# Kernel tuning notes

Hardware: AMD Instinct MI355X
Metric: run time of the kernel (lower is better)

The kernel has to match this reference:

```python
import jax, jax.numpy as jnp
import numpy as np
import math

D_MODEL, N_HEAD, N_KV_HEAD, MAX_LEN = 2048, 32, 8, 2048
D_K = D_MODEL // N_HEAD
BASE = 10000.0
B, T = 2, 2048


def _rope_tables(seq_len):
    # matches torch Rotary: cos/sin of shape [seq_len, D_K], repeat_interleave(2) over freq dim
    inv_freq = 1.0 / (BASE ** (jnp.arange(0, D_K, 2, dtype=jnp.float32) / D_K))
    t = jnp.arange(seq_len, dtype=jnp.float32)[:, None] * inv_freq  # [T, D_K/2]
    cos = jnp.repeat(jnp.cos(t), 2, axis=-1)  # [T, D_K]
    sin = jnp.repeat(jnp.sin(t), 2, axis=-1)
    return cos, sin


def _rotate_half(x):
    # faithful to source: x1 = even lanes, x2 = odd lanes, concat([-x2, x1], -1)
    x1, x2 = x[..., ::2], x[..., 1::2]
    return jnp.concatenate([-x2, x1], axis=-1)


def _apply_rope(x, cos, sin):
    return x * cos + _rotate_half(x) * sin


def setup_inputs() -> dict:
    key = jax.random.key(0)
    ks = jax.random.split(key, 5)
    s = 1.0 / math.sqrt(D_MODEL)
    x = jax.random.normal(ks[0], (B, T, D_MODEL), dtype=jnp.float32)
    Wq = jax.random.normal(ks[1], (D_MODEL, N_HEAD * D_K), dtype=jnp.float32) * s
    Wk = jax.random.normal(ks[2], (D_MODEL, N_KV_HEAD * D_K), dtype=jnp.float32) * s
    Wv = jax.random.normal(ks[3], (D_MODEL, N_KV_HEAD * D_K), dtype=jnp.float32) * s
    Wo = jax.random.normal(ks[4], (N_HEAD * D_K, D_MODEL), dtype=jnp.float32) * s
    mask = jnp.tril(jnp.ones((T, T), dtype=bool))  # causal
    return {"x": x, "mask": mask, "Wq": Wq, "Wk": Wk, "Wv": Wv, "Wo": Wo}


def reference(x, mask, Wq, Wk, Wv, Wo):
    b, t, _ = x.shape
    g = N_HEAD // N_KV_HEAD
    q = (x @ Wq).reshape(b, t, N_HEAD, D_K).transpose(0, 2, 1, 3)      # [B,H,T,d]
    k = (x @ Wk).reshape(b, t, N_KV_HEAD, D_K).transpose(0, 2, 1, 3)   # [B,Hkv,T,d]
    v = (x @ Wv).reshape(b, t, N_KV_HEAD, D_K).transpose(0, 2, 1, 3)
    cos, sin = _rope_tables(t)
    q = _apply_rope(q, cos, sin)
    k = _apply_rope(k, cos, sin)  # rope before/after repeat is identical per-head
    # grouped attention: q head h attends kv head h // g (repeat_interleave semantics)
    qg = q.reshape(b, N_KV_HEAD, g, t, D_K)
    scores = jnp.einsum("bkgtd,bksd->bkgts", qg, k) / math.sqrt(D_K)
    neg = jnp.finfo(scores.dtype).min
    scores = jnp.where(mask[None, None, None, :, :], scores, neg)
    attn = jax.nn.softmax(scores, axis=-1)
    out = jnp.einsum("bkgts,bksd->bkgtd", attn, v)
    out = out.reshape(b, N_HEAD, t, D_K).transpose(0, 2, 1, 3).reshape(b, t, N_HEAD * D_K)
    return out @ Wo
```

## Files before the change

kernel.cpp:

```cpp
#include <hip/hip_runtime.h>
#include <cstdint>
#include <cstddef>

typedef unsigned short u16;
typedef __attribute__((ext_vector_type(8))) short bf16x8;
typedef __attribute__((ext_vector_type(8))) unsigned short u16x8;
typedef __attribute__((ext_vector_type(4))) unsigned short u16x4;
typedef __attribute__((ext_vector_type(4))) float f32x4;

__device__ __forceinline__ unsigned short f2bf(float f) {
    union { float f; uint32_t u; } c; c.f = f;
    uint32_t u = c.u + 0x7fffu + ((c.u >> 16) & 1u);
    return (unsigned short)(u >> 16);
}
__device__ __forceinline__ float bf2f(unsigned short h) {
    union { uint32_t u; float f; } c; c.u = ((uint32_t)h) << 16;
    return c.f;
}
__device__ __forceinline__ uint32_t pkbf(float a, float b) {
    union { float f; uint32_t u; } x, y; x.f = a; y.f = b;
    return ((x.u + 0x8000u) >> 16) | ((y.u + 0x8000u) & 0xFFFF0000u);
}
__device__ __forceinline__ uint32_t cvtpk(float a, float b) {
    uint32_t r;
    asm("v_cvt_pk_bf16_f32 %0, %1, %2" : "=v"(r) : "v"(a), "v"(b));
    return r;
}

#define GLDS16(g, l)                                                               \
    __builtin_amdgcn_global_load_lds((const __attribute__((address_space(1))) void*)(g), \
                                     (__attribute__((address_space(3))) void*)(l), 16, 0, 0)

__global__ __launch_bounds__(256) void cvt_x(const float* __restrict__ src,
                                             u16* __restrict__ dst) {
    int i = blockIdx.x * 256 + threadIdx.x;
    const float4* s = (const float4*)src + (size_t)i * 2;
    float4 a = s[0], b = s[1];
    u16x8 o;
    o[0] = f2bf(a.x); o[1] = f2bf(a.y); o[2] = f2bf(a.z); o[3] = f2bf(a.w);
    o[4] = f2bf(b.x); o[5] = f2bf(b.y); o[6] = f2bf(b.z); o[7] = f2bf(b.w);
    *(u16x8*)(dst + (size_t)i * 8) = o;
}

__global__ __launch_bounds__(256) void tcvt(const float* __restrict__ src,
                                            u16* __restrict__ dst, int C) {
    __shared__ u16 tile[32][33];
    const int t = threadIdx.x;
    const int bx = blockIdx.x, by = blockIdx.y;
    const int tr = t >> 3, tc = (t & 7) << 2;
    float4 f = *(const float4*)&src[(size_t)(by * 32 + tr) * C + bx * 32 + tc];
    tile[tr][tc + 0] = f2bf(f.x); tile[tr][tc + 1] = f2bf(f.y);
    tile[tr][tc + 2] = f2bf(f.z); tile[tr][tc + 3] = f2bf(f.w);
    __syncthreads();
    u16x4 o;
    o[0] = tile[tc + 0][tr]; o[1] = tile[tc + 1][tr];
    o[2] = tile[tc + 2][tr]; o[3] = tile[tc + 3][tr];
    *(u16x4*)&dst[(size_t)(bx * 32 + tr) * 2048 + by * 32 + tc] = o;
}

__global__ __launch_bounds__(256) void tcvt3(const float* __restrict__ Wq,
                                             const float* __restrict__ Wk,
                                             const float* __restrict__ Wv,
                                             u16* __restrict__ dst) {
    __shared__ u16 tile[32][33];
    const int t = threadIdx.x;
    const int bxg = blockIdx.x, by = blockIdx.y;
    const float* src; int C, nb; u16* dbase;
    if (bxg < 64)      { src = Wq; C = 2048; nb = bxg;      dbase = dst; }
    else if (bxg < 80) { src = Wk; C = 512;  nb = bxg - 64; dbase = dst + (size_t)2048 * 2048; }
    else               { src = Wv; C = 512;  nb = bxg - 80; dbase = dst + (size_t)2560 * 2048; }
    const int tr = t >> 3, tc = (t & 7) << 2;
    float4 f = *(const float4*)&src[(size_t)(by * 32 + tr) * C + nb * 32 + tc];
    tile[tr][tc + 0] = f2bf(f.x); tile[tr][tc + 1] = f2bf(f.y);
    tile[tr][tc + 2] = f2bf(f.z); tile[tr][tc + 3] = f2bf(f.w);
    __syncthreads();
    u16x4 o;
    o[0] = tile[tc + 0][tr]; o[1] = tile[tc + 1][tr];
    o[2] = tile[tc + 2][tr]; o[3] = tile[tc + 3][tr];
    *(u16x4*)&dbase[(size_t)(nb * 32 + tr) * 2048 + by * 32 + tc] = o;
}

template <int MODE>
__global__ __launch_bounds__(256) void gemm2(const u16* __restrict__ A,
                                             const u16* __restrict__ Bt,
                                             u16* __restrict__ oq, u16* __restrict__ ok,
                                             u16* __restrict__ ov, float* __restrict__ of) {
    __shared__ u16 As[128 * 32];
    __shared__ u16 Bs[128 * 32];
    const int t = threadIdx.x, w = t >> 6, lane = t & 63;
    const int l15 = lane & 15, quad = lane >> 4;
    const int m0 = blockIdx.y << 7, n0 = blockIdx.x << 7;
    const int K = 2048;
    const int c0 = w * 2, c1 = c0 + 1;
    const int ar0 = c0 * 16 + (lane >> 2), ar1 = c1 * 16 + (lane >> 2);
    const int ac = (lane & 3) << 3;
    const u16* Ap0 = A + (size_t)(m0 + ar0) * K + ac;
    const u16* Ap1 = A + (size_t)(m0 + ar1) * K + ac;
    const u16* Bp0 = Bt + (size_t)(n0 + ar0) * K + ac;
    const u16* Bp1 = Bt + (size_t)(n0 + ar1) * K + ac;
    const int wm = (w >> 1) << 6, wn = (w & 1) << 6;

    f32x4 acc[4][4] = {};

    for (int k0 = 0; k0 < K; k0 += 32) {
        GLDS16(Ap0 + k0, &As[c0 * 512]);
        GLDS16(Ap1 + k0, &As[c1 * 512]);
        GLDS16(Bp0 + k0, &Bs[c0 * 512]);
        GLDS16(Bp1 + k0, &Bs[c1 * 512]);
        __syncthreads();
        bf16x8 a[4], bfr[4];
#pragma unroll
        for (int mt = 0; mt < 4; ++mt)
            a[mt] = *(bf16x8*)&As[(wm + mt * 16 + l15) * 32 + quad * 8];
#pragma unroll
        for (int nt = 0; nt < 4; ++nt)
            bfr[nt] = *(bf16x8*)&Bs[(wn + nt * 16 + l15) * 32 + quad * 8];
#pragma unroll
        for (int mt = 0; mt < 4; ++mt)
#pragma unroll
            for (int nt = 0; nt < 4; ++nt)
                acc[mt][nt] = __builtin_amdgcn_mfma_f32_16x16x32_bf16(a[mt], bfr[nt], acc[mt][nt], 0, 0, 0);
        __syncthreads();
    }

    if constexpr (MODE == 0) {
        const int colbase = n0 + wn;
        const bool isv = (colbase >= 2560);
        float iv[4];
        if (!isv) {
#pragma unroll
            for (int nt = 0; nt < 4; ++nt)
                iv[nt] = exp2f(-0.4152410118609253f * (float)(nt * 8 + (l15 >> 1)));
        }
        const int map1 = (quad << 4) | ((2 * l15 + 1) & 15);
        const int map2 = (quad << 4) | ((2 * l15) & 15);
        const bool lo = (l15 < 8);
#pragma unroll
        for (int mt = 0; mt < 4; ++mt)
#pragma unroll
            for (int r = 0; r < 4; ++r) {
                const int row = m0 + wm + mt * 16 + quad * 4 + r;
                float v0 = acc[mt][0][r], v1 = acc[mt][1][r];
                float v2 = acc[mt][2][r], v3 = acc[mt][3][r];
                float o0 = v0, o1 = v1, o2 = v2, o3 = v3;
                if (!isv) {
                    float g1a = __shfl(v0, map1), g1b = __shfl(v1, map1);
                    float g1c = __shfl(v2, map1), g1d = __shfl(v3, map1);
                    float g2a = __shfl(v0, map2), g2b = __shfl(v1, map2);
                    float g2c = __shfl(v2, map2), g2d = __shfl(v3, map2);
                    float p0 = lo ? g1a : g1b;
                    float p1 = lo ? g1c : g1d;
                    float p2 = lo ? g2a : g2b;
                    float p3 = lo ? g2c : g2d;
                    const float tt = (float)(row & 2047);
                    float sn, cs;
                    __sincosf(tt * iv[0], &sn, &cs); o0 = v0 * cs - p0 * sn;
                    __sincosf(tt * iv[1], &sn, &cs); o1 = v1 * cs - p1 * sn;
                    __sincosf(tt * iv[2], &sn, &cs); o2 = v2 * cs + p2 * sn;
                    __sincosf(tt * iv[3], &sn, &cs); o3 = v3 * cs + p3 * sn;
                }
                float o[4] = {o0, o1, o2, o3};
                if (colbase < 2048) {
#pragma unroll
                    for (int nt = 0; nt < 4; ++nt)
                        oq[(size_t)row * 2048 + colbase + nt * 16 + l15] = f2bf(o[nt]);
                } else if (colbase < 2560) {
#pragma unroll
                    for (int nt = 0; nt < 4; ++nt)
                        ok[(size_t)row * 512 + colbase - 2048 + nt * 16 + l15] = f2bf(o[nt]);
                } else {
#pragma unroll
                    for (int nt = 0; nt < 4; ++nt)
                        ov[(size_t)(colbase - 2560 + nt * 16 + l15) * 4096 + row] = f2bf(o[nt]);
                }
            }
    } else {
#pragma unroll
        for (int mt = 0; mt < 4; ++mt)
#pragma unroll
            for (int nt = 0; nt < 4; ++nt)
#pragma unroll
                for (int r = 0; r < 4; ++r) {
                    int row = m0 + wm + mt * 16 + quad * 4 + r;
                    int col = n0 + wn + nt * 16 + l15;
                    of[(size_t)row * 2048 + col] = acc[mt][nt][r];
                }
    }
}

__global__ __launch_bounds__(256, 2) void attn5(const u16* __restrict__ q,
                                                const u16* __restrict__ k,
                                                const u16* __restrict__ vT,
                                                u16* __restrict__ att) {
    __shared__ u16 Ks[64 * 72];
    __shared__ u16 Vt[64 * 72];
    __shared__ u16 Pw[4][2][2][16 * 72];

    const int t = threadIdx.x, w = t >> 6, lane = t & 63;
    const int l15 = lane & 15, quad = lane >> 4;
    const int x = blockIdx.x, kvh = blockIdx.y, z = blockIdx.z;
    const int a = z ? (31 - x) : x;
    const int h = kvh * 4 + w;
    const size_t rowbase = (size_t)z * 2048;
    const int sr = t >> 2, sd = (t & 3) << 4;
    const float SC = 0.125f * 1.4426950408889634f;

    const u16* kbase = &k[(rowbase + sr) * 512 + kvh * 64 + sd];
    const u16* vbase = &vT[(size_t)(kvh * 64 + sr) * 4096 + rowbase + sd];

    const int ntiles = a + 1;
    const int qbase0 = a * 64;

    bf16x8 aq[2][2][2];
#pragma unroll
    for (int g = 0; g < 2; ++g)
#pragma unroll
        for (int m = 0; m < 2; ++m)
#pragma unroll
            for (int kc = 0; kc < 2; ++kc)
                aq[g][m][kc] = *(const bf16x8*)&q[(rowbase + qbase0 + g * 32 + m * 16 + l15) * 2048 +
                                                  h * 64 + kc * 32 + quad * 8];

    f32x4 acc[2][2][4] = {};
    float m_i[2][2] = {{-INFINITY, -INFINITY}, {-INFINITY, -INFINITY}};
    float l_i[2][2] = {{0.f, 0.f}, {0.f, 0.f}};

    u16x8 pk0 = *(const u16x8*)kbase;
    u16x8 pk1 = *(const u16x8*)(kbase + 8);
    u16x8 pv0 = *(const u16x8*)vbase;
    u16x8 pv1 = *(const u16x8*)(vbase + 8);

    for (int kb = 0; kb < ntiles; ++kb) {
        __syncthreads();
        *(u16x8*)&Ks[sr * 72 + sd]     = pk0;
        *(u16x8*)&Ks[sr * 72 + sd + 8] = pk1;
        *(u16x8*)&Vt[sr * 72 + sd]     = pv0;
        *(u16x8*)&Vt[sr * 72 + sd + 8] = pv1;
        if (kb + 1 < ntiles) {
            const u16* kp = kbase + (size_t)(kb + 1) * 64 * 512;
            pk0 = *(const u16x8*)kp;
            pk1 = *(const u16x8*)(kp + 8);
            const u16* vp = vbase + (size_t)(kb + 1) * 64;
            pv0 = *(const u16x8*)vp;
            pv1 = *(const u16x8*)(vp + 8);
        }
        __syncthreads();

        f32x4 st[2][2][4] = {};
#pragma unroll
        for (int kt = 0; kt < 4; ++kt) {
            bf16x8 ak0 = *(bf16x8*)&Ks[(kt * 16 + l15) * 72 + quad * 8];
            bf16x8 ak1 = *(bf16x8*)&Ks[(kt * 16 + l15) * 72 + 32 + quad * 8];
#pragma unroll
            for (int g = 0; g < 2; ++g)
#pragma unroll
                for (int m = 0; m < 2; ++m) {
                    st[g][m][kt] = __builtin_amdgcn_mfma_f32_16x16x32_bf16(ak0, aq[g][m][0], st[g][m][kt], 0, 0, 0);
                    st[g][m][kt] = __builtin_amdgcn_mfma_f32_16x16x32_bf16(ak1, aq[g][m][1], st[g][m][kt], 0, 0, 0);
                }
        }
        const bool diag = (kb == ntiles - 1);

        float alpha_[2][2];
        bool  resc[2][2];
#pragma unroll
        for (int g = 0; g < 2; ++g)
#pragma unroll
            for (int m = 0; m < 2; ++m) {
                float sv[16];
#pragma unroll
                for (int kt = 0; kt < 4; ++kt)
#pragma unroll
                    for (int r = 0; r < 4; ++r) sv[kt * 4 + r] = st[g][m][kt][r];
                if (diag) {
                    const int qg = qbase0 + g * 32 + m * 16 + l15;
#pragma unroll
                    for (int kt = 0; kt < 4; ++kt)
#pragma unroll
                        for (int r = 0; r < 4; ++r) {
                            int key = kb * 64 + kt * 16 + quad * 4 + r;
                            if (key > qg) sv[kt * 4 + r] = -INFINITY;
                        }
                }
                float mx = sv[0];
#pragma unroll
                for (int i = 1; i < 16; ++i) mx = fmaxf(mx, sv[i]);
                mx = fmaxf(mx, __shfl_xor(mx, 16));
                mx = fmaxf(mx, __shfl_xor(mx, 32));
                mx *= SC;
                const float mold = m_i[g][m];
                const bool need = __any(mx > mold + 8.f);
                float al = 1.f;
                if (need) {
                    const float mnew = fmaxf(mold, mx);
                    al = __builtin_amdgcn_exp2f(mold - mnew);
                    m_i[g][m] = mnew;
                }
                const float mu = m_i[g][m];
                float sum = 0.f;
#pragma unroll
                for (int i = 0; i < 16; ++i) {
                    sv[i] = __builtin_amdgcn_exp2f(fmaf(sv[i], SC, -mu));
                    sum += sv[i];
                }
                sum += __shfl_xor(sum, 16);
                sum += __shfl_xor(sum, 32);
                l_i[g][m] = l_i[g][m] * al + sum;
                alpha_[g][m] = al;
                resc[g][m] = need;

                u16* Pq = &Pw[w][g][m][0];
#pragma unroll
                for (int kt = 0; kt < 4; ++kt) {
                    uint2 uu;
                    uu.x = cvtpk(sv[kt * 4 + 0], sv[kt * 4 + 1]);
                    uu.y = cvtpk(sv[kt * 4 + 2], sv[kt * 4 + 3]);
                    *(uint2*)&Pq[l15 * 72 + kt * 16 + quad * 4] = uu;
                }
            }

#pragma unroll
        for (int g = 0; g < 2; ++g)
#pragma unroll
            for (int m = 0; m < 2; ++m)
                if (resc[g][m]) {
                    const float al = alpha_[g][m];
#pragma unroll
                    for (int dt = 0; dt < 4; ++dt)
#pragma unroll
                        for (int r = 0; r < 4; ++r) acc[g][m][dt][r] *= al;
                }

        bf16x8 bp[2][2][2];
#pragma unroll
        for (int g = 0; g < 2; ++g)
#pragma unroll
            for (int m = 0; m < 2; ++m) {
                const u16* Pq = &Pw[w][g][m][0];
                bp[g][m][0] = *(bf16x8*)&Pq[l15 * 72 + quad * 8];
                bp[g][m][1] = *(bf16x8*)&Pq[l15 * 72 + 32 + quad * 8];
            }

#pragma unroll
        for (int dt = 0; dt < 4; ++dt) {
            bf16x8 av0 = *(bf16x8*)&Vt[(dt * 16 + l15) * 72 + quad * 8];
            bf16x8 av1 = *(bf16x8*)&Vt[(dt * 16 + l15) * 72 + 32 + quad * 8];
#pragma unroll
            for (int g = 0; g < 2; ++g)
#pragma unroll
                for (int m = 0; m < 2; ++m) {
                    acc[g][m][dt] = __builtin_amdgcn_mfma_f32_16x16x32_bf16(av0, bp[g][m][0], acc[g][m][dt], 0, 0, 0);
                    acc[g][m][dt] = __builtin_amdgcn_mfma_f32_16x16x32_bf16(av1, bp[g][m][1], acc[g][m][dt], 0, 0, 0);
                }
        }
    }

#pragma unroll
    for (int g = 0; g < 2; ++g)
#pragma unroll
        for (int m = 0; m < 2; ++m) {
            float inv = 1.0f / l_i[g][m];
            size_t row = rowbase + qbase0 + g * 32 + m * 16 + l15;
#pragma unroll
            for (int dt = 0; dt < 4; ++dt) {
                uint2 uu;
                uu.x = cvtpk(acc[g][m][dt][0] * inv, acc[g][m][dt][1] * inv);
                uu.y = cvtpk(acc[g][m][dt][2] * inv, acc[g][m][dt][3] * inv);
                *(uint2*)&att[row * 2048 + h * 64 + dt * 16 + quad * 4] = uu;
            }
        }
}

extern "C" void kernel_launch(void* const* d_in, const int* in_sizes, int n_in,
                              void* d_out, int out_size, void* d_ws, size_t ws_size,
                              hipStream_t stream) {
    const float* x  = (const float*)d_in[0];
    const float* Wq = (const float*)d_in[2];
    const float* Wk = (const float*)d_in[3];
    const float* Wv = (const float*)d_in[4];
    const float* Wo = (const float*)d_in[5];
    float* out = (float*)d_out;

    u16* xb = (u16*)d_out;

    u16* q     = (u16*)d_ws;
    u16* kk    = q + (size_t)4096 * 2048;
    u16* vt    = kk + (size_t)4096 * 512;
    u16* wqkvt = vt + (size_t)4096 * 512;
    u16* att   = wqkvt;
    u16* wot   = kk;

    cvt_x<<<4096, 256, 0, stream>>>(x, xb);
    tcvt3<<<dim3(96, 64), 256, 0, stream>>>(Wq, Wk, Wv, wqkvt);
    gemm2<0><<<dim3(24, 32), 256, 0, stream>>>(xb, wqkvt, q, kk, vt, nullptr);
    attn5<<<dim3(32, 8, 2), 256, 0, stream>>>(q, kk, vt, att);
    tcvt<<<dim3(64, 64), 256, 0, stream>>>(Wo, wot, 2048);
    gemm2<1><<<dim3(16, 32), 256, 0, stream>>>(att, wot, nullptr, nullptr, nullptr, out);
}
```

Baseline: 331.4 us.

## Double-buffer K/V in attention with 8 waves, XOR-swizzled LDS and MFMA priority

The attention kernel now runs 512 threads per block, so 8 waves each own 32 query rows instead of 4 waves owning 64. K/V tiles go into double-buffered LDS, and the next tile is stored during softmax, which drops one barrier per iteration. Padded 72-stride LDS rows are replaced by 64-wide rows with an XOR swizzle to avoid bank conflicts, and s_setprio raises priority around the MFMA sections. Per-wave register use falls, allowing more resident waves, at the cost of more LDS per block and more Q loads per block.

```diff
diff --git a/kernel.cpp b/kernel.cpp
--- a/kernel.cpp
+++ b/kernel.cpp
@@ -16,10 +16,6 @@
 __device__ __forceinline__ float bf2f(unsigned short h) {
     union { uint32_t u; float f; } c; c.u = ((uint32_t)h) << 16;
     return c.f;
-}
-__device__ __forceinline__ uint32_t pkbf(float a, float b) {
-    union { float f; uint32_t u; } x, y; x.f = a; y.f = b;
-    return ((x.u + 0x8000u) >> 16) | ((y.u + 0x8000u) & 0xFFFF0000u);
 }
 __device__ __forceinline__ uint32_t cvtpk(float a, float b) {
     uint32_t r;
@@ -188,187 +184,187 @@
     }
 }
 
-__global__ __launch_bounds__(256, 2) void attn5(const u16* __restrict__ q,
+__global__ __launch_bounds__(512, 4) void attn6(const u16* __restrict__ q,
                                                 const u16* __restrict__ k,
                                                 const u16* __restrict__ vT,
                                                 u16* __restrict__ att) {
-    __shared__ u16 Ks[64 * 72];
-    __shared__ u16 Vt[64 * 72];
-    __shared__ u16 Pw[4][2][2][16 * 72];
+    __shared__ u16 Ks[2][64 * 64];
+    __shared__ u16 Vt[2][64 * 64];
+    __shared__ u16 Pw[8][2][16 * 64];
 
     const int t = threadIdx.x, w = t >> 6, lane = t & 63;
     const int l15 = lane & 15, quad = lane >> 4;
     const int x = blockIdx.x, kvh = blockIdx.y, z = blockIdx.z;
     const int a = z ? (31 - x) : x;
-    const int h = kvh * 4 + w;
+    const int h = kvh * 4 + (w & 3);
+    const int gw = w >> 2;
     const size_t rowbase = (size_t)z * 2048;
-    const int sr = t >> 2, sd = (t & 3) << 4;
     const float SC = 0.125f * 1.4426950408889634f;
-
-    const u16* kbase = &k[(rowbase + sr) * 512 + kvh * 64 + sd];
-    const u16* vbase = &vT[(size_t)(kvh * 64 + sr) * 4096 + rowbase + sd];
+    const int swz = l15 & 7;
+
+    const int srow = t >> 3;
+    const int slot = t & 7;
+    const int sd = slot << 3;
+    const int lidx = srow * 64 + ((slot ^ (srow & 7)) << 3);
+
+    const u16* kbase = &k[(rowbase + srow) * 512 + kvh * 64 + sd];
+    const u16* vbase = &vT[(size_t)(kvh * 64 + srow) * 4096 + rowbase + sd];
 
     const int ntiles = a + 1;
-    const int qbase0 = a * 64;
-
-    bf16x8 aq[2][2][2];
-#pragma unroll
-    for (int g = 0; g < 2; ++g)
+    const int qrow0 = a * 64 + gw * 32;
+
+    bf16x8 aq[2][2];
+#pragma unroll
+    for (int m = 0; m < 2; ++m)
+#pragma unroll
+        for (int kc = 0; kc < 2; ++kc)
+            aq[m][kc] = *(const bf16x8*)&q[(rowbase + qrow0 + m * 16 + l15) * 2048 +
+                                           h * 64 + kc * 32 + quad * 8];
+
+    f32x4 acc[2][4] = {};
+    float m_i[2] = {-INFINITY, -INFINITY};
+    float l_i[2] = {0.f, 0.f};
+
+    u16x8 pk = *(const u16x8*)kbase;
+    u16x8 pv = *(const u16x8*)vbase;
+    *(u16x8*)&Ks[0][lidx] = pk;
+    *(u16x8*)&Vt[0][lidx] = pv;
+    if (ntiles > 1) {
+        pk = *(const u16x8*)(kbase + (size_t)64 * 512);
+        pv = *(const u16x8*)(vbase + 64);
+    }
+    __syncthreads();
+
+    for (int kb = 0; kb < ntiles; ++kb) {
+        const int cur = kb & 1;
+        const u16* KsC = &Ks[cur][0];
+        const u16* VtC = &Vt[cur][0];
+
+        f32x4 st[2][4] = {};
+        __builtin_amdgcn_s_setprio(1);
+#pragma unroll
+        for (int kt = 0; kt < 4; ++kt) {
+            bf16x8 ak0 = *(const bf16x8*)&KsC[(kt * 16 + l15) * 64 + ((quad ^ swz) << 3)];
+            bf16x8 ak1 = *(const bf16x8*)&KsC[(kt * 16 + l15) * 64 + (((quad + 4) ^ swz) << 3)];
+#pragma unroll
+            for (int m = 0; m < 2; ++m) {
+                st[m][kt] = __builtin_amdgcn_mfma_f32_16x16x32_bf16(ak0, aq[m][0], st[m][kt], 0, 0, 0);
+                st[m][kt] = __builtin_amdgcn_mfma_f32_16x16x32_bf16(ak1, aq[m][1], st[m][kt], 0, 0, 0);
+            }
+        }
+        __builtin_amdgcn_s_setprio(0);
+
+        const bool diag = (kb == ntiles - 1);
+        float alpha_[2];
+        bool resc[2];
+#pragma unroll
+        for (int m = 0; m < 2; ++m) {
+            float sv[16];
+#pragma unroll
+            for (int kt = 0; kt < 4; ++kt)
+#pragma unroll
+                for (int r = 0; r < 4; ++r) sv[kt * 4 + r] = st[m][kt][r];
+            if (diag) {
+                const int qg = qrow0 + m * 16 + l15;
+#pragma unroll
+                for (int kt = 0; kt < 4; ++kt)
+#pragma unroll
+                    for (int r = 0; r < 4; ++r) {
+                        int key = kb * 64 + kt * 16 + quad * 4 + r;
+                        if (key > qg) sv[kt * 4 + r] = -INFINITY;
+                    }
+            }
+            float mx = sv[0];
+#pragma unroll
+            for (int i = 1; i < 16; ++i) mx = fmaxf(mx, sv[i]);
+            mx = fmaxf(mx, __shfl_xor(mx, 16));
+            mx = fmaxf(mx, __shfl_xor(mx, 32));
+            mx *= SC;
+            const float mold = m_i[m];
+            const bool need = __any(mx > mold + 8.f);
+            float al = 1.f;
+            if (need) {
+                const float mnew = fmaxf(mold, mx);
+                al = __builtin_amdgcn_exp2f(mold - mnew);
+                m_i[m] = mnew;
+            }
+            const float mu = m_i[m];
+            float sum = 0.f;
+#pragma unroll
+            for (int i = 0; i < 16; ++i) {
+                sv[i] = __builtin_amdgcn_exp2f(fmaf(sv[i], SC, -mu));
+                sum += sv[i];
+            }
+            sum += __shfl_xor(sum, 16);
+            sum += __shfl_xor(sum, 32);
+            l_i[m] = l_i[m] * al + sum;
+            alpha_[m] = al;
+            resc[m] = need;
+
+            u16* Pq = &Pw[w][m][0];
+#pragma unroll
+            for (int kt = 0; kt < 4; ++kt) {
+                uint2 uu;
+                uu.x = cvtpk(sv[kt * 4 + 0], sv[kt * 4 + 1]);
+                uu.y = cvtpk(sv[kt * 4 + 2], sv[kt * 4 + 3]);
+                *(uint2*)&Pq[l15 * 64 + (((2 * kt + (quad >> 1)) ^ swz) << 3) + ((quad & 1) << 2)] = uu;
+            }
+        }
+
+        if (kb + 1 < ntiles) {
+            *(u16x8*)&Ks[cur ^ 1][lidx] = pk;
+            *(u16x8*)&Vt[cur ^ 1][lidx] = pv;
+            if (kb + 2 < ntiles) {
+                pk = *(const u16x8*)(kbase + (size_t)(kb + 2) * 64 * 512);
+                pv = *(const u16x8*)(vbase + (size_t)(kb + 2) * 64);
+            }
+        }
+
 #pragma unroll
         for (int m = 0; m < 2; ++m)
-#pragma unroll
-            for (int kc = 0; kc < 2; ++kc)
-                aq[g][m][kc] = *(const bf16x8*)&q[(rowbase + qbase0 + g * 32 + m * 16 + l15) * 2048 +
-                                                  h * 64 + kc * 32 + quad * 8];
-
-    f32x4 acc[2][2][4] = {};
-    float m_i[2][2] = {{-INFINITY, -INFINITY}, {-INFINITY, -INFINITY}};
-    float l_i[2][2] = {{0.f, 0.f}, {0.f, 0.f}};
-
-    u16x8 pk0 = *(const u16x8*)kbase;
-    u16x8 pk1 = *(const u16x8*)(kbase + 8);
-    u16x8 pv0 = *(const u16x8*)vbase;
-    u16x8 pv1 = *(const u16x8*)(vbase + 8);
-
-    for (int kb = 0; kb < ntiles; ++kb) {
+            if (resc[m]) {
+                const float al = alpha_[m];
+#pragma unroll
+                for (int dt = 0; dt < 4; ++dt)
+#pragma unroll
+                    for (int r = 0; r < 4; ++r) acc[m][dt][r] *= al;
+            }
+
+        bf16x8 bp[2][2];
+#pragma unroll
+        for (int m = 0; m < 2; ++m) {
+            const u16* Pq = &Pw[w][m][0];
+            bp[m][0] = *(const bf16x8*)&Pq[l15 * 64 + ((quad ^ swz) << 3)];
+            bp[m][1] = *(const bf16x8*)&Pq[l15 * 64 + (((quad + 4) ^ swz) << 3)];
+        }
+
+        __builtin_amdgcn_s_setprio(1);
+#pragma unroll
+        for (int dt = 0; dt < 4; ++dt) {
+            bf16x8 av0 = *(const bf16x8*)&VtC[(dt * 16 + l15) * 64 + ((quad ^ swz) << 3)];
+            bf16x8 av1 = *(const bf16x8*)&VtC[(dt * 16 + l15) * 64 + (((quad + 4) ^ swz) << 3)];
+#pragma unroll
+            for (int m = 0; m < 2; ++m) {
+                acc[m][dt] = __builtin_amdgcn_mfma_f32_16x16x32_bf16(av0, bp[m][0], acc[m][dt], 0, 0, 0);
+                acc[m][dt] = __builtin_amdgcn_mfma_f32_16x16x32_bf16(av1, bp[m][1], acc[m][dt], 0, 0, 0);
+            }
+        }
+        __builtin_amdgcn_s_setprio(0);
         __syncthreads();
-        *(u16x8*)&Ks[sr * 72 + sd]     = pk0;
-        *(u16x8*)&Ks[sr * 72 + sd + 8] = pk1;
-        *(u16x8*)&Vt[sr * 72 + sd]     = pv0;
-        *(u16x8*)&Vt[sr * 72 + sd + 8] = pv1;
-        if (kb + 1 < ntiles) {
-            const u16* kp = kbase + (size_t)(kb + 1) * 64 * 512;
-            pk0 = *(const u16x8*)kp;
-            pk1 = *(const u16x8*)(kp + 8);
-            const u16* vp = vbase + (size_t)(kb + 1) * 64;
-            pv0 = *(const u16x8*)vp;
-            pv1 = *(const u16x8*)(vp + 8);
-        }
-        __syncthreads();
-
-        f32x4 st[2][2][4] = {};
-#pragma unroll
-        for (int kt = 0; kt < 4; ++kt) {
-            bf16x8 ak0 = *(bf16x8*)&Ks[(kt * 16 + l15) * 72 + quad * 8];
-            bf16x8 ak1 = *(bf16x8*)&Ks[(kt * 16 + l15) * 72 + 32 + quad * 8];
-#pragma unroll
-            for (int g = 0; g < 2; ++g)
-#pragma unroll
-                for (int m = 0; m < 2; ++m) {
-                    st[g][m][kt] = __builtin_amdgcn_mfma_f32_16x16x32_bf16(ak0, aq[g][m][0], st[g][m][kt], 0, 0, 0);
-                    st[g][m][kt] = __builtin_amdgcn_mfma_f32_16x16x32_bf16(ak1, aq[g][m][1], st[g][m][kt], 0, 0, 0);
-                }
-        }
-        const bool diag = (kb == ntiles - 1);
-
-        float alpha_[2][2];
-        bool  resc[2][2];
-#pragma unroll
-        for (int g = 0; g < 2; ++g)
-#pragma unroll
-            for (int m = 0; m < 2; ++m) {
-                float sv[16];
-#pragma unroll
-                for (int kt = 0; kt < 4; ++kt)
-#pragma unroll
-                    for (int r = 0; r < 4; ++r) sv[kt * 4 + r] = st[g][m][kt][r];
-                if (diag) {
-                    const int qg = qbase0 + g * 32 + m * 16 + l15;
-#pragma unroll
-                    for (int kt = 0; kt < 4; ++kt)
-#pragma unroll
-                        for (int r = 0; r < 4; ++r) {
-                            int key = kb * 64 + kt * 16 + quad * 4 + r;
-                            if (key > qg) sv[kt * 4 + r] = -INFINITY;
-                        }
-                }
-                float mx = sv[0];
-#pragma unroll
-                for (int i = 1; i < 16; ++i) mx = fmaxf(mx, sv[i]);
-                mx = fmaxf(mx, __shfl_xor(mx, 16));
-                mx = fmaxf(mx, __shfl_xor(mx, 32));
-                mx *= SC;
-                const float mold = m_i[g][m];
-                const bool need = __any(mx > mold + 8.f);
-                float al = 1.f;
-                if (need) {
-                    const float mnew = fmaxf(mold, mx);
-                    al = __builtin_amdgcn_exp2f(mold - mnew);
-                    m_i[g][m] = mnew;
-                }
-                const float mu = m_i[g][m];
-                float sum = 0.f;
-#pragma unroll
-                for (int i = 0; i < 16; ++i) {
-                    sv[i] = __builtin_amdgcn_exp2f(fmaf(sv[i], SC, -mu));
-                    sum += sv[i];
-                }
-                sum += __shfl_xor(sum, 16);
-                sum += __shfl_xor(sum, 32);
-                l_i[g][m] = l_i[g][m] * al + sum;
-                alpha_[g][m] = al;
-                resc[g][m] = need;
-
-                u16* Pq = &Pw[w][g][m][0];
-#pragma unroll
-                for (int kt = 0; kt < 4; ++kt) {
-                    uint2 uu;
-                    uu.x = cvtpk(sv[kt * 4 + 0], sv[kt * 4 + 1]);
-                    uu.y = cvtpk(sv[kt * 4 + 2], sv[kt * 4 + 3]);
-                    *(uint2*)&Pq[l15 * 72 + kt * 16 + quad * 4] = uu;
-                }
-            }
-
-#pragma unroll
-        for (int g = 0; g < 2; ++g)
-#pragma unroll
-            for (int m = 0; m < 2; ++m)
-                if (resc[g][m]) {
-                    const float al = alpha_[g][m];
-#pragma unroll
-                    for (int dt = 0; dt < 4; ++dt)
-#pragma unroll
-                        for (int r = 0; r < 4; ++r) acc[g][m][dt][r] *= al;
-                }
-
-        bf16x8 bp[2][2][2];
-#pragma unroll
-        for (int g = 0; g < 2; ++g)
-#pragma unroll
-            for (int m = 0; m < 2; ++m) {
-                const u16* Pq = &Pw[w][g][m][0];
-                bp[g][m][0] = *(bf16x8*)&Pq[l15 * 72 + quad * 8];
-                bp[g][m][1] = *(bf16x8*)&Pq[l15 * 72 + 32 + quad * 8];
-            }
-
+    }
+
+#pragma unroll
+    for (int m = 0; m < 2; ++m) {
+        float inv = 1.0f / l_i[m];
+        size_t row = rowbase + qrow0 + m * 16 + l15;
 #pragma unroll
         for (int dt = 0; dt < 4; ++dt) {
-            bf16x8 av0 = *(bf16x8*)&Vt[(dt * 16 + l15) * 72 + quad * 8];
-            bf16x8 av1 = *(bf16x8*)&Vt[(dt * 16 + l15) * 72 + 32 + quad * 8];
-#pragma unroll
-            for (int g = 0; g < 2; ++g)
-#pragma unroll
-                for (int m = 0; m < 2; ++m) {
-                    acc[g][m][dt] = __builtin_amdgcn_mfma_f32_16x16x32_bf16(av0, bp[g][m][0], acc[g][m][dt], 0, 0, 0);
-                    acc[g][m][dt] = __builtin_amdgcn_mfma_f32_16x16x32_bf16(av1, bp[g][m][1], acc[g][m][dt], 0, 0, 0);
-                }
-        }
-    }
-
-#pragma unroll
-    for (int g = 0; g < 2; ++g)
-#pragma unroll
-        for (int m = 0; m < 2; ++m) {
-            float inv = 1.0f / l_i[g][m];
-            size_t row = rowbase + qbase0 + g * 32 + m * 16 + l15;
-#pragma unroll
-            for (int dt = 0; dt < 4; ++dt) {
-                uint2 uu;
-                uu.x = cvtpk(acc[g][m][dt][0] * inv, acc[g][m][dt][1] * inv);
-                uu.y = cvtpk(acc[g][m][dt][2] * inv, acc[g][m][dt][3] * inv);
-                *(uint2*)&att[row * 2048 + h * 64 + dt * 16 + quad * 4] = uu;
-            }
-        }
+            uint2 uu;
+            uu.x = cvtpk(acc[m][dt][0] * inv, acc[m][dt][1] * inv);
+            uu.y = cvtpk(acc[m][dt][2] * inv, acc[m][dt][3] * inv);
+            *(uint2*)&att[row * 2048 + h * 64 + dt * 16 + quad * 4] = uu;
+        }
+    }
 }
 
 extern "C" void kernel_launch(void* const* d_in, const int* in_sizes, int n_in,
@@ -393,7 +389,7 @@
     cvt_x<<<4096, 256, 0, stream>>>(x, xb);
     tcvt3<<<dim3(96, 64), 256, 0, stream>>>(Wq, Wk, Wv, wqkvt);
     gemm2<0><<<dim3(24, 32), 256, 0, stream>>>(xb, wqkvt, q, kk, vt, nullptr);
-    attn5<<<dim3(32, 8, 2), 256, 0, stream>>>(q, kk, vt, att);
+    attn6<<<dim3(32, 8, 2), 512, 0, stream>>>(q, kk, vt, att);
     tcvt<<<dim3(64, 64), 256, 0, stream>>>(Wo, wot, 2048);
     gemm2<1><<<dim3(16, 32), 256, 0, stream>>>(att, wot, nullptr, nullptr, nullptr, out);
 }
```

After: 353.4 us. 1.07x slower.
